# Kernel tuning notes

Hardware: AMD Instinct MI355X
Metric: run time of the kernel (lower is better)

## Reference

```python
import jax, jax.numpy as jnp
import numpy as np

K = 3            # kernel size
C_IN = 8
C_OUT = 16
PATCH = C_IN * K * K  # 72
EPS = 1e-6


def setup_inputs() -> dict:
    key = jax.random.key(0)
    k1, k2, k3 = jax.random.split(key, 3)
    in_tensor = jax.random.normal(k1, (4, C_IN, 112, 112), dtype=jnp.float32)
    # 1x1-conv weighting predictor: C_in -> PATCH*C_OUT channels
    w_pred = jax.random.normal(k2, (PATCH * C_OUT, C_IN), dtype=jnp.float32) * 0.05
    b_pred = jax.random.normal(k3, (PATCH * C_OUT,), dtype=jnp.float32) * 0.05
    return {"in_tensor": in_tensor, "w_pred": w_pred, "b_pred": b_pred}


def reference(in_tensor, w_pred, b_pred):
    B, C, H, W = in_tensor.shape
    # --- weighting module: predict dynamic weights per spatial location ---
    raw = jnp.einsum('bchw,oc->bohw', in_tensor, w_pred) + b_pred[None, :, None, None]
    weightings = raw.reshape(B, PATCH, C_OUT, H, W)          # [B, C*k*k, C_out, H, W]
    # norm = L2 norm of the dynamic weight over the patch dim -> [B, C_out, H, W]
    norm = jnp.sqrt(jnp.sum(weightings * weightings, axis=1)) + EPS
    # --- unfold: overlapping k x k patches, same padding, stride 1 ---
    patches = jax.lax.conv_general_dilated_patches(
        in_tensor, (K, K), (1, 1), 'SAME')                   # [B, C*k*k, H, W]
    # --- weighted sum over the patch dim, then normalize ---
    activations = jnp.einsum('bphw,bpohw->bohw', patches, weightings)  # [B, C_out, H, W]
    return activations / norm
```

## Files before the change

### kernel.cpp

```cpp
#include <hip/hip_runtime.h>
#include <math.h>

#define IMG_W 112
#define HW    12544
#define CI    8
#define CO    16
#define NP2   36
#define EPS   1e-6f

typedef __attribute__((ext_vector_type(8))) short short8;
typedef __attribute__((ext_vector_type(16))) float f32x16;

static __device__ inline short f2bf(float f) {
  unsigned u = __float_as_uint(f);
  return (short)((u + 0x7FFFu + ((u >> 16) & 1u)) >> 16);
}

static constexpr int DQ[9] = {-113, -112, -111, -1, 0, 1, 111, 112, 113};

__global__ __launch_bounds__(256) void coda_pack(
    const float* __restrict__ wp, const float* __restrict__ bp,
    short* __restrict__ wpk)
{
  const int t = blockIdx.x * 256 + threadIdx.x;
  if (t >= NP2 * 64) return;
  const int p2 = t >> 6, l = t & 63, ah = l >> 5, m = l & 31;
  const int row = p2 * 32 + m;
  short8 v = {0, 0, 0, 0, 0, 0, 0, 0};
  if (ah == 0) {
    const float* wr = wp + row * CI;
#pragma unroll
    for (int j = 0; j < 8; ++j) v[j] = f2bf(wr[j]);
  } else {
    v[0] = f2bf(bp[row]);
  }
  *(short8*)&wpk[t * 8] = v;
}

__global__ __launch_bounds__(256, 4) void coda_mfma(
    const float* __restrict__ in, const short* __restrict__ wpk,
    float* __restrict__ out)
{
  __shared__ float sPart[2 * 16 * 64];

  const int tid = threadIdx.x;
  const int b   = blockIdx.x / 196;
  const int r0  = (blockIdx.x - b * 196) * 64;
  const float* __restrict__ inb = in + b * CI * HW;

  const int wave = tid >> 6;
  const int lane = tid & 63;
  const int g    = wave & 1;
  const int hh   = wave >> 1;
  const int ln   = lane & 31;
  const int hi   = lane >> 5;
  const int px   = r0 + g * 32 + ln;
  const int hrow = px / IMG_W;
  const int wcol = px - hrow * IMG_W;

  float vm[9];
#pragma unroll
  for (int q = 0; q < 9; ++q) {
    const int kh = q / 3, kw = q % 3;
    const bool ok = ((unsigned)(hrow + kh - 1) < 112u) &&
                    ((unsigned)(wcol + kw - 1) < 112u);
    vm[q] = ok ? 1.f : 0.f;
  }

  short8 bf;
#pragma unroll
  for (int j = 0; j < 8; ++j) {
    const short bv = f2bf(inb[j * HW + px]);
    bf[j] = (hi == 0) ? bv : ((j == 0) ? (short)0x3F80 : (short)0);
  }

  float acc[8] = {0.f, 0.f, 0.f, 0.f, 0.f, 0.f, 0.f, 0.f};
  float n2[8]  = {0.f, 0.f, 0.f, 0.f, 0.f, 0.f, 0.f, 0.f};

  const short* __restrict__ wbase = wpk + (hh * 18 * 64 + lane) * 8;

#pragma unroll
  for (int t = 0; t < 18; ++t) {
    const int p0  = 36 * hh + 2 * t;
    const int c0_ = p0 / 9,       q0_ = p0 % 9;
    const int c1_ = (p0 + 1) / 9, q1_ = (p0 + 1) % 9;

    const short8 af = *(const short8*)(wbase + t * 512);

    int i0 = px + DQ[q0_]; i0 = i0 < 0 ? 0 : (i0 > HW - 1 ? HW - 1 : i0);
    int i1 = px + DQ[q1_]; i1 = i1 < 0 ? 0 : (i1 > HW - 1 ? HW - 1 : i1);
    const float pv0 = vm[q0_] * inb[c0_ * HW + i0];
    const float pv1 = vm[q1_] * inb[c1_ * HW + i1];

    const f32x16 zc = {0.f, 0.f, 0.f, 0.f, 0.f, 0.f, 0.f, 0.f,
                       0.f, 0.f, 0.f, 0.f, 0.f, 0.f, 0.f, 0.f};
    const f32x16 d =
        __builtin_amdgcn_mfma_f32_32x32x16_bf16(af, bf, zc, 0, 0, 0);
#pragma unroll
    for (int i = 0; i < 16; ++i) {
      const float pv = (i < 8) ? pv0 : pv1;
      acc[i & 7] = fmaf(pv, d[i], acc[i & 7]);
      n2[i & 7]  = fmaf(d[i], d[i], n2[i & 7]);
    }
  }

  if (hh == 1) {
#pragma unroll
    for (int j = 0; j < 8; ++j) {
      sPart[(g * 16 + j) * 64 + lane]     = acc[j];
      sPart[(g * 16 + j + 8) * 64 + lane] = n2[j];
    }
  }
  __syncthreads();
  if (hh == 0) {
    float* __restrict__ ob = out + (long)b * CO * HW + px;
#pragma unroll
    for (int j = 0; j < 8; ++j) {
      const float a2 = acc[j] + sPart[(g * 16 + j) * 64 + lane];
      const float s2 = n2[j] + sPart[(g * 16 + j + 8) * 64 + lane];
      const int co = (j & 3) + 8 * (j >> 2) + 4 * hi;
      ob[(long)co * HW] = a2 / (sqrtf(s2) + EPS);
    }
  }
}

extern "C" void kernel_launch(void* const* d_in, const int* in_sizes, int n_in,
                              void* d_out, int out_size, void* d_ws, size_t ws_size,
                              hipStream_t stream) {
  const float* in = (const float*)d_in[0];
  const float* wp = (const float*)d_in[1];
  const float* bp = (const float*)d_in[2];
  float* out = (float*)d_out;
  short* wpk = (short*)d_ws;

  coda_pack<<<dim3(9), dim3(256), 0, stream>>>(wp, bp, wpk);
  coda_mfma<<<dim3(784), dim3(256), 0, stream>>>(in, wpk, out);
}
```

Baseline: 72.60 us.

## Split patch reduction across four wave pairs per block instead of two

```diff
diff --git a/kernel.cpp b/kernel.cpp
--- a/kernel.cpp
+++ b/kernel.cpp
@@ -37,11 +37,11 @@
   *(short8*)&wpk[t * 8] = v;
 }
 
-__global__ __launch_bounds__(256, 4) void coda_mfma(
+__global__ __launch_bounds__(512, 6) void coda_mfma(
     const float* __restrict__ in, const short* __restrict__ wpk,
     float* __restrict__ out)
 {
-  __shared__ float sPart[2 * 16 * 64];
+  __shared__ float sPart[6 * 1024];
 
   const int tid = threadIdx.x;
   const int b   = blockIdx.x / 196;
@@ -51,7 +51,7 @@
   const int wave = tid >> 6;
   const int lane = tid & 63;
   const int g    = wave & 1;
-  const int hh   = wave >> 1;
+  const int qh   = wave >> 1;
   const int ln   = lane & 31;
   const int hi   = lane >> 5;
   const int px   = r0 + g * 32 + ln;
@@ -77,13 +77,14 @@
   float acc[8] = {0.f, 0.f, 0.f, 0.f, 0.f, 0.f, 0.f, 0.f};
   float n2[8]  = {0.f, 0.f, 0.f, 0.f, 0.f, 0.f, 0.f, 0.f};
 
-  const short* __restrict__ wbase = wpk + (hh * 18 * 64 + lane) * 8;
+  const short* __restrict__ wbase = wpk + (qh * 9 * 64 + lane) * 8;
 
 #pragma unroll
-  for (int t = 0; t < 18; ++t) {
-    const int p0  = 36 * hh + 2 * t;
-    const int c0_ = p0 / 9,       q0_ = p0 % 9;
-    const int c1_ = (p0 + 1) / 9, q1_ = (p0 + 1) % 9;
+  for (int t = 0; t < 9; ++t) {
+    const int q0_ = (2 * t) % 9;
+    const int q1_ = (2 * t + 1) % 9;
+    const int c0_ = 2 * qh + (2 * t) / 9;
+    const int c1_ = 2 * qh + (2 * t + 1) / 9;
 
     const short8 af = *(const short8*)(wbase + t * 512);
 
@@ -104,20 +105,26 @@
     }
   }
 
-  if (hh == 1) {
+  if (qh != 0) {
+    const int slot = ((qh - 1) * 2 + g) * 1024;
 #pragma unroll
     for (int j = 0; j < 8; ++j) {
-      sPart[(g * 16 + j) * 64 + lane]     = acc[j];
-      sPart[(g * 16 + j + 8) * 64 + lane] = n2[j];
+      sPart[slot + j * 64 + lane]       = acc[j];
+      sPart[slot + (8 + j) * 64 + lane] = n2[j];
     }
   }
   __syncthreads();
-  if (hh == 0) {
+  if (qh == 0) {
     float* __restrict__ ob = out + (long)b * CO * HW + px;
 #pragma unroll
     for (int j = 0; j < 8; ++j) {
-      const float a2 = acc[j] + sPart[(g * 16 + j) * 64 + lane];
-      const float s2 = n2[j] + sPart[(g * 16 + j + 8) * 64 + lane];
+      float a2 = acc[j];
+      float s2 = n2[j];
+#pragma unroll
+      for (int u = 0; u < 3; ++u) {
+        a2 += sPart[(u * 2 + g) * 1024 + j * 64 + lane];
+        s2 += sPart[(u * 2 + g) * 1024 + (8 + j) * 64 + lane];
+      }
       const int co = (j & 3) + 8 * (j >> 2) + 4 * hi;
       ob[(long)co * HW] = a2 / (sqrtf(s2) + EPS);
     }
@@ -134,5 +141,5 @@
   short* wpk = (short*)d_ws;
 
   coda_pack<<<dim3(9), dim3(256), 0, stream>>>(wp, bp, wpk);
-  coda_mfma<<<dim3(784), dim3(256), 0, stream>>>(in, wpk, out);
+  coda_mfma<<<dim3(784), dim3(512), 0, stream>>>(in, wpk, out);
 }
```

Measured after the change: 67.38 us (median of 2 runs). 7.2% less time.
